# Kernel optimization log

Hardware: AMD Instinct MI355X
Metric: run time of the kernel (lower is better)

Reference implementation:

```python
import jax, jax.numpy as jnp
import numpy as np

GAMMA = 1.0  # rbf kernel bandwidth (config.gamma)
LN_EPS = 1e-5


def _layernorm(x, w):
    # LayerNorm(d_embed, bias=False): normalize last dim, scale by w
    mu = jnp.mean(x, axis=-1, keepdims=True)
    var = jnp.var(x, axis=-1, keepdims=True)
    return (x - mu) * jax.lax.rsqrt(var + LN_EPS) * w


def setup_inputs() -> dict:
    key = jax.random.key(0)
    ks = jax.random.split(key, 8)
    B, S, D, H = 4, 1024, 256, 8
    x = jax.random.normal(ks[0], (B, S, D), dtype=jnp.float32)
    e = jax.random.normal(ks[1], (B, S, D), dtype=jnp.float32)
    p = jax.random.normal(ks[2], (B, S, D), dtype=jnp.float32)
    W_q = 0.02 * jax.random.normal(ks[3], (H, D, D), dtype=jnp.float32)
    W_k = 0.02 * jax.random.normal(ks[4], (H, D, D), dtype=jnp.float32)
    W_v = 0.02 * jax.random.normal(ks[5], (H, D, D), dtype=jnp.float32)
    n_layer = 12
    W_o = (0.02 / np.sqrt(2 * n_layer)) * jax.random.normal(ks[6], (H * D, D), dtype=jnp.float32)
    ln_w = jnp.ones((D,), dtype=jnp.float32)
    return {"x": x, "e": e, "p": p, "W_q": W_q, "W_k": W_k, "W_v": W_v, "W_o": W_o, "ln_w": ln_w}


def reference(x, e, p, W_q, W_k, W_v, W_o, ln_w):
    # use_ppe=False path: only x is used (e, p ignored)
    B, S, D = x.shape
    H = W_q.shape[0]
    xn = _layernorm(x, ln_w)                                   # [B,S,D]
    # per-head full-size projections: Q/K/V [B,H,S,D]
    Q = jnp.einsum('bsd,hde->bhse', xn, W_q)
    K = jnp.einsum('bsd,hde->bhse', xn, W_k)
    V = jnp.einsum('bsd,hde->bhse', xn, W_v)
    # rbf kernel: exp(-gamma * ||q-k||^2) via the expansion trick
    q2 = jnp.sum(Q * Q, axis=-1)                               # [B,H,S]
    k2 = jnp.sum(K * K, axis=-1)                               # [B,H,S]
    qk = jnp.einsum('bhse,bhte->bhst', Q, K)                   # [B,H,S,S]
    dist2 = jnp.maximum(q2[..., :, None] + k2[..., None, :] - 2.0 * qk, 0.0)
    attn = jnp.exp(-GAMMA * dist2)                             # [B,H,S,S]
    # nto=True -> no causal mask; dropout=0 (eval) -> identity
    out = jnp.einsum('bhst,bhte->bhse', attn, V)               # [B,H,S,D]
    out = jnp.swapaxes(out, 1, 2).reshape(B, S, H * D)         # concat heads
    return out @ W_o                                           # [B,S,D]
```

## Files before the change

### kernel.cpp

```cpp
#include <hip/hip_runtime.h>
#include <cstdint>
#include <cstddef>

#define B_ 4
#define S_ 1024
#define D_ 256
#define H_ 8

typedef unsigned short u16;
typedef __attribute__((ext_vector_type(8))) short short8v;
typedef __attribute__((ext_vector_type(8))) _Float16 half8v;
typedef __attribute__((ext_vector_type(4))) float f32x4;
typedef __attribute__((ext_vector_type(4))) u16 u16x4;
typedef __attribute__((ext_vector_type(8))) u16 u16x8;

__device__ inline u16 f2b(float f) {
  unsigned u = __builtin_bit_cast(unsigned, f);
  unsigned r = (u + 0x7FFFu + ((u >> 16) & 1u)) >> 16;
  return (u16)r;
}
__device__ inline float b2f(u16 h) {
  return __builtin_bit_cast(float, ((unsigned)h) << 16);
}
__device__ inline u16 f2h(float f) {
  return __builtin_bit_cast(u16, (_Float16)f);
}
__device__ inline f32x4 mfma16(short8v a, short8v b, f32x4 c) {
  return __builtin_amdgcn_mfma_f32_16x16x32_bf16(a, b, c, 0, 0, 0);
}
__device__ inline f32x4 mfma16h(half8v a, half8v b, f32x4 c) {
  return __builtin_amdgcn_mfma_f32_16x16x32_f16(a, b, c, 0, 0, 0);
}
__device__ __forceinline__ void gl16(const u16* g, u16* l) {
  __builtin_amdgcn_global_load_lds((const uint32_t*)g, (uint32_t*)l, 16, 0, 0);
}

__global__ __launch_bounds__(256) void lnwt_kernel(
    const float* __restrict__ x, const float* __restrict__ w,
    const float* __restrict__ Wq, const float* __restrict__ Wk,
    const float* __restrict__ Wv, const float* __restrict__ Wo,
    u16* __restrict__ xf, u16* __restrict__ WTf, u16* __restrict__ WoTf,
    float* __restrict__ k2) {
  const int bid = blockIdx.x;
  const int tid = threadIdx.x;
  if (bid < 1024) {
    const int wid = tid >> 6, lane = tid & 63;
    const int row = bid * 4 + wid;
    const float4 v4 = *reinterpret_cast<const float4*>(x + (size_t)row * D_ + lane * 4);
    const float4 w4 = *reinterpret_cast<const float4*>(w + lane * 4);
    float s  = v4.x + v4.y + v4.z + v4.w;
    float s2 = v4.x * v4.x + v4.y * v4.y + v4.z * v4.z + v4.w * v4.w;
#pragma unroll
    for (int off = 1; off < 64; off <<= 1) {
      s  += __shfl_xor(s, off);
      s2 += __shfl_xor(s2, off);
    }
    const float mu  = s * (1.0f / D_);
    const float var = s2 * (1.0f / D_) - mu * mu;
    const float rr  = rsqrtf(var + 1e-5f);
    u16x4 o;
    o[0] = f2h((v4.x - mu) * rr * w4.x);
    o[1] = f2h((v4.y - mu) * rr * w4.y);
    o[2] = f2h((v4.z - mu) * rr * w4.z);
    o[3] = f2h((v4.w - mu) * rr * w4.w);
    *reinterpret_cast<u16x4*>(xf + (size_t)row * D_ + lane * 4) = o;
  } else if (bid >= 1536) {
    const size_t i = ((size_t)(bid - 1536) * 256 + tid) * 8;
    const float4 z4 = {0.f, 0.f, 0.f, 0.f};
    *reinterpret_cast<float4*>(k2 + i)     = z4;
    *reinterpret_cast<float4*>(k2 + i + 4) = z4;
  } else {
    __shared__ float t[32][33];
    const int tc = tid & 31, tr = tid >> 5;
    const int zb = (bid - 1024) * 4;
#pragma unroll
    for (int i = 0; i < 4; ++i) {
      const int z = zb + i;
      if (i) __syncthreads();
      if (z < 1536) {
        const int wm = z >> 6;
        const int mat = wm >> 3, h = wm & 7;
        const float* src = (mat == 0 ? Wq : mat == 1 ? Wk : Wv) + (size_t)h * 65536;
        const int t6 = z & 63;
        const int r0 = (t6 >> 3) * 32, c0 = (t6 & 7) * 32;
#pragma unroll
        for (int k = 0; k < 4; ++k)
          t[tr + k * 8][tc] = src[(size_t)(r0 + tr + k * 8) * 256 + c0 + tc];
        __syncthreads();
        u16* df = WTf + (size_t)wm * 65536;
#pragma unroll
        for (int k = 0; k < 4; ++k) {
          const float v = t[tc][tr + k * 8];
          df[(size_t)(c0 + tr + k * 8) * 256 + r0 + tc] = f2h(v);
        }
      } else {
        const int z2 = z - 1536;
        const int r0 = (z2 >> 3) * 32, c0 = (z2 & 7) * 32;
#pragma unroll
        for (int k = 0; k < 4; ++k)
          t[tr + k * 8][tc] = Wo[(size_t)(r0 + tr + k * 8) * 256 + c0 + tc];
        __syncthreads();
#pragma unroll
        for (int k = 0; k < 4; ++k) {
          const float v = t[tc][tr + k * 8];
          WoTf[(size_t)(c0 + tr + k * 8) * 2048 + r0 + tc] = f2b(v);
        }
      }
    }
  }
}

__global__ __launch_bounds__(256, 3) void proj_kernel(
    const u16* __restrict__ xf, const u16* __restrict__ WTf,
    u16* __restrict__ Qf, u16* __restrict__ Kf,
    u16* __restrict__ Vt, float* __restrict__ k2g) {
  const int z = blockIdx.y;
  const int mat = z >> 3, h = z & 7;
  const int xb = blockIdx.x;

  const u16 *Ap, *Bp;
  int arow0, brow0;
  if (mat < 2) {
    Ap = WTf + (size_t)z * 65536; arow0 = (xb >> 5) * 128;
    Bp = xf;                      brow0 = (xb & 31) * 128;
  } else {
    Ap = xf;                      arow0 = (xb & 31) * 128;
    Bp = WTf + (size_t)z * 65536; brow0 = (xb >> 5) * 128;
  }

  __shared__ u16 LS[2 * 128 * 64];
  u16* AS = LS; u16* BS = LS + 128 * 64;
  char* LSb = (char*)LS;
  char* ASb = (char*)AS; char* BSb = (char*)BS;

  const int tid = threadIdx.x;
  const int w = tid >> 6, lane = tid & 63;
  const int lr = lane & 15, lh = lane >> 4;
  const int wm = w >> 1, wn = w & 1;

  f32x4 acc[4][4];
#pragma unroll
  for (int i = 0; i < 4; ++i)
#pragma unroll
    for (int j = 0; j < 4; ++j) acc[i][j] = (f32x4){0.f, 0.f, 0.f, 0.f};

  for (int k0 = 0; k0 < 256; k0 += 64) {
    __syncthreads();
#pragma unroll
    for (int j = 0; j < 4; ++j) {
      const int c0 = j * 256 + w * 64;
      const int c = c0 + lane;
      const int m = c >> 3, sl = c & 7;
      const int l = sl ^ (m & 7);
      gl16(Ap + (size_t)(arow0 + m) * 256 + k0 + l * 8, AS + c0 * 8);
    }
#pragma unroll
    for (int j = 0; j < 4; ++j) {
      const int c0 = j * 256 + w * 64;
      const int c = c0 + lane;
      const int n = c >> 3, sl = c & 7;
      const int l = sl ^ (n & 7);
      gl16(Bp + (size_t)(brow0 + n) * 256 + k0 + l * 8, BS + c0 * 8);
    }
    __syncthreads();

#pragma unroll
    for (int ks = 0; ks < 2; ++ks) {
      half8v af[4], bf[4];
#pragma unroll
      for (int mf = 0; mf < 4; ++mf) {
        const int m = wm * 64 + mf * 16 + lr;
        af[mf] = *reinterpret_cast<const half8v*>(
            ASb + m * 128 + (((ks * 4 + lh) * 16) ^ ((m & 7) << 4)));
      }
#pragma unroll
      for (int nf = 0; nf < 4; ++nf) {
        const int n = wn * 64 + nf * 16 + lr;
        bf[nf] = *reinterpret_cast<const half8v*>(
            BSb + n * 128 + (((ks * 4 + lh) * 16) ^ ((n & 7) << 4)));
      }
      __builtin_amdgcn_s_setprio(1);
#pragma unroll
      for (int mf = 0; mf < 4; ++mf)
#pragma unroll
        for (int nf = 0; nf < 4; ++nf)
          acc[mf][nf] = mfma16h(af[mf], bf[nf], acc[mf][nf]);
      __builtin_amdgcn_s_setprio(0);
    }
  }

  __syncthreads();

  if (mat < 2) {
    u16* Hf = (mat == 0) ? Qf : Kf;
#pragma unroll
    for (int mf = 0; mf < 4; ++mf)
#pragma unroll
      for (int nf = 0; nf < 4; ++nf) {
        const int sl_ = wn * 64 + nf * 16 + lr;
        const int el_ = wm * 64 + mf * 16 + lh * 4;
        u16x4 hv;
#pragma unroll
        for (int r = 0; r < 4; ++r) hv[r] = f2h(acc[mf][nf][r]);
        *reinterpret_cast<u16x4*>(LSb + sl_ * 256 + ((el_ * 2) ^ ((sl_ & 7) << 4))) = hv;
      }
    if (mat == 1) {
#pragma unroll
      for (int nf = 0; nf < 4; ++nf) {
        float p = 0.f;
#pragma unroll
        for (int mf = 0; mf < 4; ++mf)
#pragma unroll
          for (int r = 0; r < 4; ++r) {
            const float v = (float)(_Float16)acc[mf][nf][r];
            p = fmaf(v, v, p);
          }
        p += __shfl_xor(p, 16);
        p += __shfl_xor(p, 32);
        if (lh == 0) {
          const int s = brow0 + wn * 64 + nf * 16 + lr;
          const int bb = s >> 10;
          atomicAdd(&k2g[(size_t)(bb * H_ + h) * S_ + (s & 1023)], p);
        }
      }
    }
    __syncthreads();
#pragma unroll
    for (int i = 0; i < 8; ++i) {
      const int c = i * 256 + tid;
      const int sl_ = c >> 4, ch = c & 15;
      const u16x8 v = *reinterpret_cast<const u16x8*>(
          LSb + sl_ * 256 + ((ch * 16) ^ ((sl_ & 7) << 4)));
      const int s = brow0 + sl_;
      const int bb = s >> 10;
      *reinterpret_cast<u16x8*>(
          Hf + ((size_t)(bb * H_ + h) * S_ + (s & 1023)) * D_ + arow0 + ch * 8) = v;
    }
  } else {
#pragma unroll
    for (int mf = 0; mf < 4; ++mf)
#pragma unroll
      for (int nf = 0; nf < 4; ++nf) {
        const int dl_ = wn * 64 + nf * 16 + lr;
        const int sl_ = wm * 64 + mf * 16 + lh * 4;
        u16x4 hv;
#pragma unroll
        for (int r = 0; r < 4; ++r) hv[r] = f2b(acc[mf][nf][r]);
        *reinterpret_cast<u16x4*>(LSb + dl_ * 256 + ((sl_ * 2) ^ ((dl_ & 7) << 4))) = hv;
      }
    __syncthreads();
#pragma unroll
    for (int i = 0; i < 8; ++i) {
      const int c = i * 256 + tid;
      const int dl_ = c >> 4, ch = c & 15;
      const u16x8 v = *reinterpret_cast<const u16x8*>(
          LSb + dl_ * 256 + ((ch * 16) ^ ((dl_ & 7) << 4)));
      const int d = brow0 + dl_;
      const int sg = arow0 + ch * 8;
      const int bb = sg >> 10;
      *reinterpret_cast<u16x8*>(
          Vt + ((size_t)(bb * H_ + h) * D_ + d) * S_ + (sg & 1023)) = v;
    }
  }
}

__global__ __launch_bounds__(256, 2) void attn_kernel(
    const u16* __restrict__ Qf, const u16* __restrict__ Kf,
    const u16* __restrict__ Vt, const float* __restrict__ k2,
    u16* __restrict__ aOf) {
  const int bh  = blockIdx.x;
  const int qt  = blockIdx.y;
  const int tid = threadIdx.x;
  const int w = tid >> 6, lane = tid & 63;
  const int lr = lane & 15, lh = lane >> 4;
  const int qg = w >> 1, kvh = w & 1;

  __shared__ u16 KS[64 * 256];
  __shared__ u16 VS[256 * 64];
  __shared__ u16 PS[64 * 64];
  __shared__ float K2S[1024];
  char* KB = (char*)KS; char* VB = (char*)VS; char* PB = (char*)PS;

  half8v qf[2][8];
#pragma unroll
  for (int at = 0; at < 2; ++at) {
    const int qrow = qt * 64 + qg * 32 + at * 16 + lr;
    const size_t qbase = ((size_t)(bh * S_) + qrow) * D_ + lh * 8;
#pragma unroll
    for (int ds = 0; ds < 8; ++ds)
      qf[at][ds] = *reinterpret_cast<const half8v*>(Qf + qbase + ds * 32);
  }

  const size_t kgbase = (size_t)(bh * S_);
  const size_t vgbase = (size_t)(bh * D_);

#pragma unroll
  for (int j = 0; j < 8; ++j) {
    const int c0 = j * 256 + w * 64;
    const int c = c0 + lane;
    const int row = c >> 5, slot = c & 31;
    gl16(Kf + (kgbase + row) * D_ + ((slot ^ (row & 7)) << 3), KS + c0 * 8);
  }
  gl16((const u16*)(k2 + (size_t)bh * S_) + tid * 8, (u16*)K2S + tid * 8);
#pragma unroll
  for (int j = 0; j < 8; ++j) {
    const int c0 = j * 256 + w * 64;
    const int c = c0 + lane;
    const int d = c >> 3, slot = c & 7;
    gl16(Vt + (vgbase + d) * S_ + ((slot ^ (d & 7)) << 3), VS + c0 * 8);
  }

  float q2v[2];
#pragma unroll
  for (int at = 0; at < 2; ++at) {
    float p = 0.f;
#pragma unroll
    for (int ds = 0; ds < 8; ++ds)
#pragma unroll
      for (int j = 0; j < 8; ++j) {
        const float v = (float)qf[at][ds][j];
        p = fmaf(v, v, p);
      }
    p += __shfl_xor(p, 16);
    p += __shfl_xor(p, 32);
    q2v[at] = p;
  }

  asm volatile("s_waitcnt vmcnt(8)" ::: "memory");
  __builtin_amdgcn_sched_barrier(0);
  __builtin_amdgcn_s_barrier();

  f32x4 oacc[4][4];
#pragma unroll
  for (int i = 0; i < 4; ++i)
#pragma unroll
    for (int j = 0; j < 4; ++j) oacc[i][j] = (f32x4){0.f, 0.f, 0.f, 0.f};

  for (int kt = 0; kt < 16; ++kt) {
    const int last = (kt == 15);

    asm volatile("s_waitcnt vmcnt(8)" ::: "memory");
    __builtin_amdgcn_sched_barrier(0);

    f32x4 k2v[2];
#pragma unroll
    for (int bt = 0; bt < 2; ++bt)
      k2v[bt] = *reinterpret_cast<const f32x4*>(
          K2S + kt * 64 + kvh * 32 + bt * 16 + lh * 4);

    f32x4 pacc[2][2];
#pragma unroll
    for (int at = 0; at < 2; ++at)
#pragma unroll
      for (int bt = 0; bt < 2; ++bt) pacc[at][bt] = (f32x4){0.f, 0.f, 0.f, 0.f};
#pragma unroll
    for (int ds = 0; ds < 8; ++ds) {
      half8v kf[2];
#pragma unroll
      for (int bt = 0; bt < 2; ++bt) {
        const int krow = kvh * 32 + bt * 16 + lr;
        kf[bt] = *reinterpret_cast<const half8v*>(
            KB + krow * 512 + (((ds * 64) + lh * 16) ^ ((krow & 7) << 4)));
      }
      __builtin_amdgcn_s_setprio(1);
#pragma unroll
      for (int at = 0; at < 2; ++at)
#pragma unroll
        for (int bt = 0; bt < 2; ++bt)
          pacc[at][bt] = mfma16h(kf[bt], qf[at][ds], pacc[at][bt]);
      __builtin_amdgcn_s_setprio(0);
    }

#pragma unroll
    for (int at = 0; at < 2; ++at) {
      const int q = qg * 32 + at * 16 + lr;
#pragma unroll
      for (int bt = 0; bt < 2; ++bt) {
        const int kv0 = kvh * 32 + bt * 16 + lh * 4;
        u16x4 pv;
#pragma unroll
        for (int r = 0; r < 4; ++r) {
          float d2 = q2v[at] + k2v[bt][r] - 2.0f * pacc[at][bt][r];
          d2 = fmaxf(d2, 0.f);
          pv[r] = f2b(__expf(-d2));
        }
        *reinterpret_cast<u16x4*>(PB + q * 128 + ((kv0 * 2) ^ ((q & 7) << 4))) = pv;
      }
    }
    asm volatile("s_waitcnt vmcnt(0) lgkmcnt(0)" ::: "memory");
    __builtin_amdgcn_sched_barrier(0);
    __builtin_amdgcn_s_barrier();

    if (!last) {
#pragma unroll
      for (int j = 0; j < 8; ++j) {
        const int c0 = j * 256 + w * 64;
        const int c = c0 + lane;
        const int row = c >> 5, slot = c & 31;
        gl16(Kf + (kgbase + (kt + 1) * 64 + row) * D_ + ((slot ^ (row & 7)) << 3),
             KS + c0 * 8);
      }
    }

    short8v vfr[4][2];
#pragma unroll
    for (int dt = 0; dt < 4; ++dt)
#pragma unroll
      for (int ks = 0; ks < 2; ++ks) {
        const int d = w * 64 + dt * 16 + lr;
        vfr[dt][ks] = *reinterpret_cast<const short8v*>(
            VB + d * 128 + (((ks * 64) + lh * 16) ^ ((d & 7) << 4)));
      }
#pragma unroll
    for (int pq = 0; pq < 4; ++pq) {
      short8v pa[2];
#pragma unroll
      for (int ks = 0; ks < 2; ++ks) {
        const int q = pq * 16 + lr;
        pa[ks] = *reinterpret_cast<const short8v*>(
            PB + q * 128 + (((ks * 64) + lh * 16) ^ ((q & 7) << 4)));
      }
      __builtin_amdgcn_s_setprio(1);
#pragma unroll
      for (int dt = 0; dt < 4; ++dt) {
        oacc[pq][dt] = mfma16(pa[0], vfr[dt][0], oacc[pq][dt]);
        oacc[pq][dt] = mfma16(pa[1], vfr[dt][1], oacc[pq][dt]);
      }
      __builtin_amdgcn_s_setprio(0);
    }
    if (!last) {
      asm volatile("s_waitcnt lgkmcnt(0)" ::: "memory");
      __builtin_amdgcn_sched_barrier(0);
      __builtin_amdgcn_s_barrier();

#pragma unroll
      for (int j = 0; j < 8; ++j) {
        const int c0 = j * 256 + w * 64;
        const int c = c0 + lane;
        const int d = c >> 3, slot = c & 7;
        gl16(Vt + (vgbase + d) * S_ + (kt + 1) * 64 + ((slot ^ (d & 7)) << 3),
             VS + c0 * 8);
      }
    }
  }

  const int bb = bh >> 3, hh = bh & 7;
#pragma unroll
  for (int pq = 0; pq < 4; ++pq)
#pragma unroll
    for (int dt = 0; dt < 4; ++dt)
#pragma unroll
      for (int r = 0; r < 4; ++r) {
        const int s = qt * 64 + pq * 16 + lh * 4 + r;
        const int d = w * 64 + dt * 16 + lr;
        const size_t idx = ((size_t)(bb * S_) + s) * (H_ * D_) + hh * D_ + d;
        aOf[idx] = f2b(oacc[pq][dt][r]);
      }
}

__global__ __launch_bounds__(512, 4) void outproj_kernel(
    const u16* __restrict__ WoTf, const u16* __restrict__ aOf,
    u16* __restrict__ pbuf) {
  const int xb = blockIdx.x;
  const int kc = blockIdx.y;
  const int bm = xb >> 5, bn = xb & 31;
  const int arow0 = bm * 128, brow0 = bn * 128;

  __shared__ u16 AhS[128 * 64], BhS[128 * 64];
  char* AhB = (char*)AhS; char* BhB = (char*)BhS;

  const int tid = threadIdx.x;
  const int w = tid >> 6, lane = tid & 63;
  const int lr = lane & 15, lh = lane >> 4;
  const int wr = w >> 2, wc = w & 3;

  f32x4 acc[4][2];
#pragma unroll
  for (int i = 0; i < 4; ++i)
#pragma unroll
    for (int j = 0; j < 2; ++j) acc[i][j] = (f32x4){0.f, 0.f, 0.f, 0.f};

  for (int k0 = kc * 512; k0 < kc * 512 + 512; k0 += 64) {
#pragma unroll
    for (int i = 0; i < 2; ++i) {
      const int c = tid + i * 512;
      const int row = c >> 3, slot = c & 7;
      const int off = row * 128 + ((slot * 16) ^ ((row & 7) << 4));
      const size_t ga = (size_t)(arow0 + row) * 2048 + k0 + slot * 8;
      const size_t gb = (size_t)(brow0 + row) * 2048 + k0 + slot * 8;
      *reinterpret_cast<short8v*>(AhB + off) = *reinterpret_cast<const short8v*>(WoTf + ga);
      *reinterpret_cast<short8v*>(BhB + off) = *reinterpret_cast<const short8v*>(aOf + gb);
    }
    __syncthreads();
#pragma unroll
    for (int ks = 0; ks < 2; ++ks) {
      short8v afh[4], bfh[2];
#pragma unroll
      for (int mf = 0; mf < 4; ++mf) {
        const int m = wr * 64 + mf * 16 + lr;
        afh[mf] = *reinterpret_cast<const short8v*>(
            AhB + m * 128 + (((ks * 64) + lh * 16) ^ ((m & 7) << 4)));
      }
#pragma unroll
      for (int nf = 0; nf < 2; ++nf) {
        const int n = wc * 32 + nf * 16 + lr;
        bfh[nf] = *reinterpret_cast<const short8v*>(
            BhB + n * 128 + (((ks * 64) + lh * 16) ^ ((n & 7) << 4)));
      }
      __builtin_amdgcn_s_setprio(1);
#pragma unroll
      for (int mf = 0; mf < 4; ++mf)
#pragma unroll
        for (int nf = 0; nf < 2; ++nf)
          acc[mf][nf] = mfma16(afh[mf], bfh[nf], acc[mf][nf]);
      __builtin_amdgcn_s_setprio(0);
    }
    __syncthreads();
  }

  u16* pout = pbuf + (size_t)kc * (4096 * 256);
#pragma unroll
  for (int mf = 0; mf < 4; ++mf) {
    const int e0 = bm * 128 + wr * 64 + mf * 16 + lh * 4;
#pragma unroll
    for (int nf = 0; nf < 2; ++nf) {
      const int s = bn * 128 + wc * 32 + nf * 16 + lr;
      u16x4 hv;
#pragma unroll
      for (int r = 0; r < 4; ++r) hv[r] = f2b(acc[mf][nf][r]);
      *reinterpret_cast<u16x4*>(pout + (size_t)s * D_ + e0) = hv;
    }
  }
}

__global__ __launch_bounds__(256) void reduce_kernel(const u16* __restrict__ pbuf,
                                                     float* __restrict__ out) {
  const size_t i = ((size_t)blockIdx.x * 256 + threadIdx.x) * 8;
  const size_t C = (size_t)4096 * 256;
  const u16x8 a = *reinterpret_cast<const u16x8*>(pbuf + i);
  const u16x8 b = *reinterpret_cast<const u16x8*>(pbuf + C + i);
  const u16x8 c = *reinterpret_cast<const u16x8*>(pbuf + 2 * C + i);
  const u16x8 d = *reinterpret_cast<const u16x8*>(pbuf + 3 * C + i);
  float4 o0, o1;
#pragma unroll
  for (int j = 0; j < 8; ++j) {
    const float v = b2f((u16)a[j]) + b2f((u16)b[j]) + b2f((u16)c[j]) + b2f((u16)d[j]);
    if (j < 4) (&o0.x)[j] = v; else (&o1.x)[j - 4] = v;
  }
  *reinterpret_cast<float4*>(out + i)     = o0;
  *reinterpret_cast<float4*>(out + i + 4) = o1;
}

extern "C" void kernel_launch(void* const* d_in, const int* in_sizes, int n_in,
                              void* d_out, int out_size, void* d_ws, size_t ws_size,
                              hipStream_t stream) {
  (void)in_sizes; (void)n_in; (void)out_size; (void)ws_size;
  const float* x   = (const float*)d_in[0];
  const float* Wq  = (const float*)d_in[3];
  const float* Wk  = (const float*)d_in[4];
  const float* Wv  = (const float*)d_in[5];
  const float* Wo  = (const float*)d_in[6];
  const float* lnw = (const float*)d_in[7];
  float* out = (float*)d_out;

  char* ws = (char*)d_ws;
  u16*  xf   = (u16*)(ws);
  u16*  WTf  = (u16*)(ws + ((size_t)2   << 20));
  u16*  WoTf = (u16*)(ws + ((size_t)5   << 20));
  float* k2  = (float*)(ws + ((size_t)6  << 20));
  u16*  Qf   = (u16*)(ws + ((size_t)8   << 20));
  u16*  Kf   = (u16*)(ws + ((size_t)24  << 20));
  u16*  Vt   = (u16*)(ws + ((size_t)40  << 20));
  u16*  aOf  = (u16*)(ws + ((size_t)56  << 20));
  u16*  pbuf = (u16*)(ws + ((size_t)72  << 20));

  lnwt_kernel<<<dim3(1552), dim3(256), 0, stream>>>(x, lnw, Wq, Wk, Wv, Wo, xf, WTf, WoTf, k2);
  proj_kernel<<<dim3(64, 24), dim3(256), 0, stream>>>(xf, WTf, Qf, Kf, Vt, k2);
  attn_kernel<<<dim3(32, 16), dim3(256), 0, stream>>>(Qf, Kf, Vt, k2, aOf);
  outproj_kernel<<<dim3(64, 4), dim3(512), 0, stream>>>(WoTf, aOf, pbuf);
  reduce_kernel<<<dim3(512), dim3(256), 0, stream>>>(pbuf, out);
}
```

Measured before the change: 89.76 us.

## Replace split-K out-projection and reduce pass with single full-K GEMM

The out-projection moves from a 4-way split-K with bf16 partial buffers plus a separate reduce kernel to a single kernel that runs over the whole 2048-long K dimension. Each block computes a 64x64 output tile in 128-wide K steps and writes fp32 directly. Tiles are loaded with gl16 direct-to-LDS loads. This removes the partial-buffer write/read traffic and one kernel launch. In exchange there are fewer, longer blocks (256 total), smaller tiles with less reuse, and no double buffering, so load latency is less hidden.

```diff
diff --git a/kernel.cpp b/kernel.cpp
--- a/kernel.cpp
+++ b/kernel.cpp
@@ -458,97 +458,65 @@
       }
 }
 
-__global__ __launch_bounds__(512, 4) void outproj_kernel(
+__global__ __launch_bounds__(512, 2) void outproj_kernel(
     const u16* __restrict__ WoTf, const u16* __restrict__ aOf,
-    u16* __restrict__ pbuf) {
-  const int xb = blockIdx.x;
-  const int kc = blockIdx.y;
-  const int bm = xb >> 5, bn = xb & 31;
-  const int arow0 = bm * 128, brow0 = bn * 128;
-
-  __shared__ u16 AhS[128 * 64], BhS[128 * 64];
+    float* __restrict__ out) {
+  const int bid = blockIdx.x;
+  const int bm = bid >> 6;
+  const int bn = bid & 63;
+  const int e0t = bm * 64, s0t = bn * 64;
+
+  __shared__ u16 AhS[64 * 128], BhS[64 * 128];
   char* AhB = (char*)AhS; char* BhB = (char*)BhS;
 
   const int tid = threadIdx.x;
   const int w = tid >> 6, lane = tid & 63;
   const int lr = lane & 15, lh = lane >> 4;
-  const int wr = w >> 2, wc = w & 3;
-
-  f32x4 acc[4][2];
-#pragma unroll
-  for (int i = 0; i < 4; ++i)
-#pragma unroll
-    for (int j = 0; j < 2; ++j) acc[i][j] = (f32x4){0.f, 0.f, 0.f, 0.f};
-
-  for (int k0 = kc * 512; k0 < kc * 512 + 512; k0 += 64) {
-#pragma unroll
-    for (int i = 0; i < 2; ++i) {
-      const int c = tid + i * 512;
-      const int row = c >> 3, slot = c & 7;
-      const int off = row * 128 + ((slot * 16) ^ ((row & 7) << 4));
-      const size_t ga = (size_t)(arow0 + row) * 2048 + k0 + slot * 8;
-      const size_t gb = (size_t)(brow0 + row) * 2048 + k0 + slot * 8;
-      *reinterpret_cast<short8v*>(AhB + off) = *reinterpret_cast<const short8v*>(WoTf + ga);
-      *reinterpret_cast<short8v*>(BhB + off) = *reinterpret_cast<const short8v*>(aOf + gb);
-    }
+  const int wm = w >> 1, wn = w & 1;
+
+  f32x4 acc[2];
+  acc[0] = (f32x4){0.f, 0.f, 0.f, 0.f};
+  acc[1] = (f32x4){0.f, 0.f, 0.f, 0.f};
+
+  for (int k0 = 0; k0 < 2048; k0 += 128) {
     __syncthreads();
 #pragma unroll
-    for (int ks = 0; ks < 2; ++ks) {
-      short8v afh[4], bfh[2];
-#pragma unroll
-      for (int mf = 0; mf < 4; ++mf) {
-        const int m = wr * 64 + mf * 16 + lr;
-        afh[mf] = *reinterpret_cast<const short8v*>(
-            AhB + m * 128 + (((ks * 64) + lh * 16) ^ ((m & 7) << 4)));
-      }
+    for (int j = 0; j < 2; ++j) {
+      const int c = j * 512 + tid;
+      const int row = c >> 4, slot = c & 15;
+      const int l = slot ^ (row & 7);
+      gl16(WoTf + (size_t)(e0t + row) * 2048 + k0 + l * 8, AhS + c * 8);
+      gl16(aOf  + (size_t)(s0t + row) * 2048 + k0 + l * 8, BhS + c * 8);
+    }
+    __syncthreads();
+
+#pragma unroll
+    for (int ks = 0; ks < 4; ++ks) {
+      const int m = wm * 16 + lr;
+      const short8v afh = *reinterpret_cast<const short8v*>(
+          AhB + m * 256 + ((ks * 64 + lh * 16) ^ ((m & 7) << 4)));
+      short8v bfh[2];
 #pragma unroll
       for (int nf = 0; nf < 2; ++nf) {
-        const int n = wc * 32 + nf * 16 + lr;
+        const int n = wn * 32 + nf * 16 + lr;
         bfh[nf] = *reinterpret_cast<const short8v*>(
-            BhB + n * 128 + (((ks * 64) + lh * 16) ^ ((n & 7) << 4)));
+            BhB + n * 256 + ((ks * 64 + lh * 16) ^ ((n & 7) << 4)));
       }
       __builtin_amdgcn_s_setprio(1);
-#pragma unroll
-      for (int mf = 0; mf < 4; ++mf)
-#pragma unroll
-        for (int nf = 0; nf < 2; ++nf)
-          acc[mf][nf] = mfma16(afh[mf], bfh[nf], acc[mf][nf]);
+      acc[0] = mfma16(afh, bfh[0], acc[0]);
+      acc[1] = mfma16(afh, bfh[1], acc[1]);
       __builtin_amdgcn_s_setprio(0);
     }
-    __syncthreads();
-  }
-
-  u16* pout = pbuf + (size_t)kc * (4096 * 256);
-#pragma unroll
-  for (int mf = 0; mf < 4; ++mf) {
-    const int e0 = bm * 128 + wr * 64 + mf * 16 + lh * 4;
-#pragma unroll
-    for (int nf = 0; nf < 2; ++nf) {
-      const int s = bn * 128 + wc * 32 + nf * 16 + lr;
-      u16x4 hv;
-#pragma unroll
-      for (int r = 0; r < 4; ++r) hv[r] = f2b(acc[mf][nf][r]);
-      *reinterpret_cast<u16x4*>(pout + (size_t)s * D_ + e0) = hv;
-    }
-  }
-}
-
-__global__ __launch_bounds__(256) void reduce_kernel(const u16* __restrict__ pbuf,
-                                                     float* __restrict__ out) {
-  const size_t i = ((size_t)blockIdx.x * 256 + threadIdx.x) * 8;
-  const size_t C = (size_t)4096 * 256;
-  const u16x8 a = *reinterpret_cast<const u16x8*>(pbuf + i);
-  const u16x8 b = *reinterpret_cast<const u16x8*>(pbuf + C + i);
-  const u16x8 c = *reinterpret_cast<const u16x8*>(pbuf + 2 * C + i);
-  const u16x8 d = *reinterpret_cast<const u16x8*>(pbuf + 3 * C + i);
-  float4 o0, o1;
-#pragma unroll
-  for (int j = 0; j < 8; ++j) {
-    const float v = b2f((u16)a[j]) + b2f((u16)b[j]) + b2f((u16)c[j]) + b2f((u16)d[j]);
-    if (j < 4) (&o0.x)[j] = v; else (&o1.x)[j - 4] = v;
-  }
-  *reinterpret_cast<float4*>(out + i)     = o0;
-  *reinterpret_cast<float4*>(out + i + 4) = o1;
+  }
+
+  const int e0 = e0t + wm * 16 + lh * 4;
+#pragma unroll
+  for (int nf = 0; nf < 2; ++nf) {
+    const int s = s0t + wn * 32 + nf * 16 + lr;
+    float4 ov;
+    ov.x = acc[nf][0]; ov.y = acc[nf][1]; ov.z = acc[nf][2]; ov.w = acc[nf][3];
+    *reinterpret_cast<float4*>(out + (size_t)s * D_ + e0) = ov;
+  }
 }
 
 extern "C" void kernel_launch(void* const* d_in, const int* in_sizes, int n_in,
@@ -572,11 +540,9 @@
   u16*  Kf   = (u16*)(ws + ((size_t)24  << 20));
   u16*  Vt   = (u16*)(ws + ((size_t)40  << 20));
   u16*  aOf  = (u16*)(ws + ((size_t)56  << 20));
-  u16*  pbuf = (u16*)(ws + ((size_t)72  << 20));
 
   lnwt_kernel<<<dim3(1552), dim3(256), 0, stream>>>(x, lnw, Wq, Wk, Wv, Wo, xf, WTf, WoTf, k2);
   proj_kernel<<<dim3(64, 24), dim3(256), 0, stream>>>(xf, WTf, Qf, Kf, Vt, k2);
   attn_kernel<<<dim3(32, 16), dim3(256), 0, stream>>>(Qf, Kf, Vt, k2, aOf);
-  outproj_kernel<<<dim3(64, 4), dim3(512), 0, stream>>>(WoTf, aOf, pbuf);
-  reduce_kernel<<<dim3(512), dim3(256), 0, stream>>>(pbuf, out);
-}
+  outproj_kernel<<<dim3(256), dim3(512), 0, stream>>>(WoTf, aOf, out);
+}
```

Result: slower. 92.02 us (+2.5%).
